# Optimization experiments

Hardware: AMD Instinct MI355X
Metric: run time of the kernel (lower is better)

The kernel has to match this reference:

```python
import jax, jax.numpy as jnp
import numpy as np


def setup_inputs() -> dict:
    key = jax.random.key(0)
    k1, k2 = jax.random.split(key)
    A, B, N, M, K = 8, 16, 1024, 1024, 64
    u = jax.random.normal(k1, (A, B, N, K), dtype=jnp.float32)
    v = jax.random.normal(k2, (A, B, M, K), dtype=jnp.float32)
    return {"u": u, "v": v}


def reference(u, v):
    # to_norm = u @ v^T has shape (A,B,N,M); we only need its row/col sums.
    # sum over M of (u @ v^T) = u @ sum_m(v);  sum over N = v @ sum_n(u).
    v_sum = v.sum(axis=2)                     # (A,B,K)
    u_sum = u.sum(axis=2)                     # (A,B,K)
    row_sum = jnp.einsum('abnk,abk->abn', u, v_sum)   # to_norm.sum(dim=3)
    col_sum = jnp.einsum('abmk,abk->abm', v, u_sum)   # to_norm.sum(dim=2)
    left_mul = jax.nn.relu(jnp.sign(row_sum))[..., None]   # (A,B,N,1)
    right_mul = jax.nn.relu(jnp.sign(col_sum))[..., None]  # (A,B,M,1)
    return (left_mul * u, right_mul * v)
```

## Files before the change

### kernel.cpp

```cpp
#include <hip/hip_runtime.h>


#define NBATCH 128
#define NROW   1024
#define KDIM   64
#define ELEMS_PER_TENSOR (128ull * 1024ull * 64ull)

typedef float floatx4 __attribute__((ext_vector_type(4)));

__global__ __launch_bounds__(1024)
void fused_overlap_kernel(const float* __restrict__ u,
                          const float* __restrict__ v,
                          float* __restrict__ out) {
    const int bid   = blockIdx.x;
    const int xcd   = bid & 7;
    const int slot  = bid >> 3;
    const int batch = xcd * 16 + (slot >> 1);
    const int half  = slot & 1;
    const int tid   = threadIdx.x;
    const int k4    = tid & 15;
    const int rg    = tid >> 4;
    const int wave  = tid >> 6;

    const size_t boff = (size_t)batch * NROW * KDIM;
    const float4* ub = (const float4*)(u + boff);
    const float4* vb = (const float4*)(v + boff);
    float* ou = out + boff;
    float* ov = out + ELEMS_PER_TENSOR + boff;

    const int r_own0 = half * 512 + rg;
    const int r_oth0 = (1 - half) * 512 + rg;

    __shared__ float4 red_v[16][16];
    __shared__ float4 red_u[16][16];

    float4 vr[8];
    float4 sv = make_float4(0.f, 0.f, 0.f, 0.f);
    #pragma unroll
    for (int i = 0; i < 8; ++i) {
        size_t io = (size_t)(r_own0 + 64 * i) * 16 + k4;
        vr[i] = vb[io];
        sv.x += vr[i].x; sv.y += vr[i].y; sv.z += vr[i].z; sv.w += vr[i].w;
    }
    #pragma unroll
    for (int i = 0; i < 8; ++i) {
        size_t ix = (size_t)(r_oth0 + 64 * i) * 16 + k4;
        float4 b = vb[ix];
        sv.x += b.x; sv.y += b.y; sv.z += b.z; sv.w += b.w;
    }

    sv.x += __shfl_xor(sv.x, 16); sv.y += __shfl_xor(sv.y, 16);
    sv.z += __shfl_xor(sv.z, 16); sv.w += __shfl_xor(sv.w, 16);
    sv.x += __shfl_xor(sv.x, 32); sv.y += __shfl_xor(sv.y, 32);
    sv.z += __shfl_xor(sv.z, 32); sv.w += __shfl_xor(sv.w, 32);
    if ((tid & 63) < 16)
        red_v[wave][k4] = sv;
    __syncthreads();

    float4 vs = make_float4(0.f, 0.f, 0.f, 0.f);
    #pragma unroll
    for (int w = 0; w < 16; ++w) {
        float4 t = red_v[w][k4];
        vs.x += t.x; vs.y += t.y; vs.z += t.z; vs.w += t.w;
    }

    float4 su = make_float4(0.f, 0.f, 0.f, 0.f);
    #pragma unroll
    for (int i = 0; i < 8; ++i) {
        size_t io = (size_t)(r_own0 + 64 * i) * 16 + k4;
        float4 a = ub[io];
        su.x += a.x; su.y += a.y; su.z += a.z; su.w += a.w;
        float pu = a.x * vs.x + a.y * vs.y + a.z * vs.z + a.w * vs.w;
        pu += __shfl_xor(pu, 1);
        pu += __shfl_xor(pu, 2);
        pu += __shfl_xor(pu, 4);
        pu += __shfl_xor(pu, 8);
        float mu = (pu > 0.f) ? 1.f : 0.f;
        floatx4 outu = { a.x * mu, a.y * mu, a.z * mu, a.w * mu };
        __builtin_nontemporal_store(outu, (floatx4*)(ou + io * 4));
    }
    #pragma unroll
    for (int i = 0; i < 8; ++i) {
        size_t ix = (size_t)(r_oth0 + 64 * i) * 16 + k4;
        float4 a = ub[ix];
        su.x += a.x; su.y += a.y; su.z += a.z; su.w += a.w;
    }

    su.x += __shfl_xor(su.x, 16); su.y += __shfl_xor(su.y, 16);
    su.z += __shfl_xor(su.z, 16); su.w += __shfl_xor(su.w, 16);
    su.x += __shfl_xor(su.x, 32); su.y += __shfl_xor(su.y, 32);
    su.z += __shfl_xor(su.z, 32); su.w += __shfl_xor(su.w, 32);
    if ((tid & 63) < 16)
        red_u[wave][k4] = su;
    __syncthreads();

    float4 us = make_float4(0.f, 0.f, 0.f, 0.f);
    #pragma unroll
    for (int w = 0; w < 16; ++w) {
        float4 t = red_u[w][k4];
        us.x += t.x; us.y += t.y; us.z += t.z; us.w += t.w;
    }

    #pragma unroll
    for (int i = 0; i < 8; ++i) {
        size_t io = (size_t)(r_own0 + 64 * i) * 16 + k4;
        float pv = vr[i].x * us.x + vr[i].y * us.y + vr[i].z * us.z + vr[i].w * us.w;
        pv += __shfl_xor(pv, 1);
        pv += __shfl_xor(pv, 2);
        pv += __shfl_xor(pv, 4);
        pv += __shfl_xor(pv, 8);
        float mv = (pv > 0.f) ? 1.f : 0.f;
        floatx4 outv = { vr[i].x * mv, vr[i].y * mv, vr[i].z * mv, vr[i].w * mv };
        __builtin_nontemporal_store(outv, (floatx4*)(ov + io * 4));
    }
}

extern "C" void kernel_launch(void* const* d_in, const int* in_sizes, int n_in,
                              void* d_out, int out_size, void* d_ws, size_t ws_size,
                              hipStream_t stream) {
    const float* u = (const float*)d_in[0];
    const float* v = (const float*)d_in[1];
    float* out = (float*)d_out;

    fused_overlap_kernel<<<dim3(256), dim3(1024), 0, stream>>>(u, v, out);
}
```

Baseline: 117.9 us.

## Process each batch in one block, loading u and v once into registers

Replaces the two-blocks-per-batch split, where each block re-read the other half for the column sums, with one 1024-thread block per batch that loads all of u and v into registers. Both sums are then reduced together with a single barrier. This removes the duplicated global reads and one synchronization. In exchange the grid halves to 128 blocks, leaving many CUs idle, and register pressure rises to 32 float4 per thread.

After: 151.9 us. 1.29x slower.

```diff
diff --git a/kernel.cpp b/kernel.cpp
--- a/kernel.cpp
+++ b/kernel.cpp
@@ -9,14 +9,10 @@
 typedef float floatx4 __attribute__((ext_vector_type(4)));
 
 __global__ __launch_bounds__(1024)
-void fused_overlap_kernel(const float* __restrict__ u,
-                          const float* __restrict__ v,
-                          float* __restrict__ out) {
-    const int bid   = blockIdx.x;
-    const int xcd   = bid & 7;
-    const int slot  = bid >> 3;
-    const int batch = xcd * 16 + (slot >> 1);
-    const int half  = slot & 1;
+void fused_batch_kernel(const float* __restrict__ u,
+                        const float* __restrict__ v,
+                        float* __restrict__ out) {
+    const int batch = blockIdx.x;
     const int tid   = threadIdx.x;
     const int k4    = tid & 15;
     const int rg    = tid >> 4;
@@ -28,82 +24,61 @@
     float* ou = out + boff;
     float* ov = out + ELEMS_PER_TENSOR + boff;
 
-    const int r_own0 = half * 512 + rg;
-    const int r_oth0 = (1 - half) * 512 + rg;
-
-    __shared__ float4 red_v[16][16];
-    __shared__ float4 red_u[16][16];
-
-    float4 vr[8];
+    float4 ur[16], vr[16];
+    float4 su = make_float4(0.f, 0.f, 0.f, 0.f);
     float4 sv = make_float4(0.f, 0.f, 0.f, 0.f);
     #pragma unroll
-    for (int i = 0; i < 8; ++i) {
-        size_t io = (size_t)(r_own0 + 64 * i) * 16 + k4;
+    for (int i = 0; i < 16; ++i) {
+        size_t io = (size_t)(rg + 64 * i) * 16 + k4;
+        ur[i] = ub[io];
         vr[i] = vb[io];
-        sv.x += vr[i].x; sv.y += vr[i].y; sv.z += vr[i].z; sv.w += vr[i].w;
     }
     #pragma unroll
-    for (int i = 0; i < 8; ++i) {
-        size_t ix = (size_t)(r_oth0 + 64 * i) * 16 + k4;
-        float4 b = vb[ix];
-        sv.x += b.x; sv.y += b.y; sv.z += b.z; sv.w += b.w;
-    }
-
-    sv.x += __shfl_xor(sv.x, 16); sv.y += __shfl_xor(sv.y, 16);
-    sv.z += __shfl_xor(sv.z, 16); sv.w += __shfl_xor(sv.w, 16);
-    sv.x += __shfl_xor(sv.x, 32); sv.y += __shfl_xor(sv.y, 32);
-    sv.z += __shfl_xor(sv.z, 32); sv.w += __shfl_xor(sv.w, 32);
-    if ((tid & 63) < 16)
-        red_v[wave][k4] = sv;
-    __syncthreads();
-
-    float4 vs = make_float4(0.f, 0.f, 0.f, 0.f);
-    #pragma unroll
-    for (int w = 0; w < 16; ++w) {
-        float4 t = red_v[w][k4];
-        vs.x += t.x; vs.y += t.y; vs.z += t.z; vs.w += t.w;
-    }
-
-    float4 su = make_float4(0.f, 0.f, 0.f, 0.f);
-    #pragma unroll
-    for (int i = 0; i < 8; ++i) {
-        size_t io = (size_t)(r_own0 + 64 * i) * 16 + k4;
-        float4 a = ub[io];
-        su.x += a.x; su.y += a.y; su.z += a.z; su.w += a.w;
-        float pu = a.x * vs.x + a.y * vs.y + a.z * vs.z + a.w * vs.w;
-        pu += __shfl_xor(pu, 1);
-        pu += __shfl_xor(pu, 2);
-        pu += __shfl_xor(pu, 4);
-        pu += __shfl_xor(pu, 8);
-        float mu = (pu > 0.f) ? 1.f : 0.f;
-        floatx4 outu = { a.x * mu, a.y * mu, a.z * mu, a.w * mu };
-        __builtin_nontemporal_store(outu, (floatx4*)(ou + io * 4));
-    }
-    #pragma unroll
-    for (int i = 0; i < 8; ++i) {
-        size_t ix = (size_t)(r_oth0 + 64 * i) * 16 + k4;
-        float4 a = ub[ix];
-        su.x += a.x; su.y += a.y; su.z += a.z; su.w += a.w;
+    for (int i = 0; i < 16; ++i) {
+        su.x += ur[i].x; su.y += ur[i].y; su.z += ur[i].z; su.w += ur[i].w;
+        sv.x += vr[i].x; sv.y += vr[i].y; sv.z += vr[i].z; sv.w += vr[i].w;
     }
 
     su.x += __shfl_xor(su.x, 16); su.y += __shfl_xor(su.y, 16);
     su.z += __shfl_xor(su.z, 16); su.w += __shfl_xor(su.w, 16);
     su.x += __shfl_xor(su.x, 32); su.y += __shfl_xor(su.y, 32);
     su.z += __shfl_xor(su.z, 32); su.w += __shfl_xor(su.w, 32);
-    if ((tid & 63) < 16)
+    sv.x += __shfl_xor(sv.x, 16); sv.y += __shfl_xor(sv.y, 16);
+    sv.z += __shfl_xor(sv.z, 16); sv.w += __shfl_xor(sv.w, 16);
+    sv.x += __shfl_xor(sv.x, 32); sv.y += __shfl_xor(sv.y, 32);
+    sv.z += __shfl_xor(sv.z, 32); sv.w += __shfl_xor(sv.w, 32);
+
+    __shared__ float4 red_u[16][16];
+    __shared__ float4 red_v[16][16];
+    if ((tid & 63) < 16) {
         red_u[wave][k4] = su;
+        red_v[wave][k4] = sv;
+    }
     __syncthreads();
 
     float4 us = make_float4(0.f, 0.f, 0.f, 0.f);
+    float4 vs = make_float4(0.f, 0.f, 0.f, 0.f);
     #pragma unroll
     for (int w = 0; w < 16; ++w) {
-        float4 t = red_u[w][k4];
-        us.x += t.x; us.y += t.y; us.z += t.z; us.w += t.w;
+        float4 a = red_u[w][k4];
+        float4 b = red_v[w][k4];
+        us.x += a.x; us.y += a.y; us.z += a.z; us.w += a.w;
+        vs.x += b.x; vs.y += b.y; vs.z += b.z; vs.w += b.w;
     }
 
     #pragma unroll
-    for (int i = 0; i < 8; ++i) {
-        size_t io = (size_t)(r_own0 + 64 * i) * 16 + k4;
+    for (int i = 0; i < 16; ++i) {
+        size_t io = (size_t)(rg + 64 * i) * 16 + k4;
+
+        float pu = ur[i].x * vs.x + ur[i].y * vs.y + ur[i].z * vs.z + ur[i].w * vs.w;
+        pu += __shfl_xor(pu, 1);
+        pu += __shfl_xor(pu, 2);
+        pu += __shfl_xor(pu, 4);
+        pu += __shfl_xor(pu, 8);
+        float mu = (pu > 0.f) ? 1.f : 0.f;
+        floatx4 outu = { ur[i].x * mu, ur[i].y * mu, ur[i].z * mu, ur[i].w * mu };
+        __builtin_nontemporal_store(outu, (floatx4*)(ou + io * 4));
+
         float pv = vr[i].x * us.x + vr[i].y * us.y + vr[i].z * us.z + vr[i].w * us.w;
         pv += __shfl_xor(pv, 1);
         pv += __shfl_xor(pv, 2);
@@ -122,5 +97,5 @@
     const float* v = (const float*)d_in[1];
     float* out = (float*)d_out;
 
-    fused_overlap_kernel<<<dim3(256), dim3(1024), 0, stream>>>(u, v, out);
+    fused_batch_kernel<<<dim3(128), dim3(1024), 0, stream>>>(u, v, out);
 }
```
